# Performance work log

Hardware: AMD Instinct MI355X
Metric: run time of the kernel (lower is better)

Reference implementation:

```python
import jax, jax.numpy as jnp
import numpy as np

DEPTH = 6
N_EST = 16
IN_DIM = 512
N_CLASSES = 100
BATCH = 8192
N_NODES = 2 ** DEPTH - 1   # 63 internal nodes
N_LEAVES = 2 ** DEPTH      # 64 leaves


def entmax15(t):
    # Source's (nonstandard) entmax15: softmax(relu(t)**1.5)
    z = jax.nn.relu(t)
    return jax.nn.softmax(z ** 1.5, axis=-1)


def _leaf_paths():
    # Ancestor node index and branch bit for every (depth level j, leaf l),
    # exactly matching: idx = 2**(j-1) + l // 2**(depth-(j-1)) - 1
    #                   bit = (l // 2**(depth-j)) % 2
    l = np.arange(N_LEAVES)
    j = np.arange(1, DEPTH + 1)[:, None]
    idx = (2 ** (j - 1) + l[None, :] // (2 ** (DEPTH - (j - 1))) - 1).astype(np.int32)
    bits = ((l[None, :] // (2 ** (DEPTH - j))) % 2).astype(np.int32)
    return jnp.asarray(idx), jnp.asarray(bits)  # both (DEPTH, N_LEAVES)


def setup_inputs() -> dict:
    key = jax.random.key(0)
    kx, kT, kL = jax.random.split(key, 3)
    x = jax.random.normal(kx, (BATCH, IN_DIM), dtype=jnp.float32)
    T = jax.random.normal(kT, (N_EST, N_NODES, IN_DIM), dtype=jnp.float32)
    L = jax.random.normal(kL, (N_EST, N_LEAVES, N_CLASSES), dtype=jnp.float32)
    return {"x": x, "T": T, "L": L}


def reference(x, T, L):
    # Hard feature selection with straight-through: forward = hardmax(entmax15(T)),
    # backward = 0 (in the torch source, I = I - (I - hardmax(I)) kills the gradient).
    I_soft = entmax15(T)  # (E, N, D)
    I = jax.lax.stop_gradient(
        (I_soft == I_soft.max(axis=-1, keepdims=True)).astype(x.dtype)
    )
    # Per-node split decisions for all nodes at once.
    t_dot = jnp.einsum('end,end->en', T, I)          # (E, N) threshold value
    x_dot = jnp.einsum('bd,end->ben', x, I)          # (B, E, N) selected feature
    # s = s - (s - floor(s)) == floor(s); floor has zero gradient (matches torch).
    s = jnp.floor(t_dot[None, :, :] - x_dot)         # (B, E, N)

    idx, bits = _leaf_paths()                        # (DEPTH, N_LEAVES)
    sg = s[..., idx]                                 # (B, E, DEPTH, N_LEAVES)
    factors = jnp.where(bits[None, None] == 1, 1.0 - sg, sg)
    p = jnp.prod(factors, axis=2)                    # (B, E, N_LEAVES)

    # Leaf values, summed over the ensemble.
    y_hat = jnp.einsum('bel,elc->bc', p, L)          # (B, C)
    return jax.nn.softmax(y_hat, axis=-1)
```

## Files before the change

### kernel.cpp

```cpp
#include <hip/hip_runtime.h>
#include <hip/hip_bf16.h>
#include <math.h>

#define IN_DIM 512
#define NC 100
#define NN 63
#define NE 16
#define BATCH 8192
#define XP 516

typedef __attribute__((ext_vector_type(8))) short bf16x8;
typedef __attribute__((ext_vector_type(4))) float f32x4;

static __device__ __forceinline__ ushort bf16_bits(__hip_bfloat16 h) {
  union { __hip_bfloat16 b; ushort u; } cv; cv.b = h; return cv.u;
}

__global__ __launch_bounds__(256) void prep_kernel(
    const float* __restrict__ T, const float* __restrict__ L,
    ushort* __restrict__ Bfrag, float* __restrict__ tmax, int* __restrict__ dstar) {
  const int tid = threadIdx.x;
  const int bid = blockIdx.x;

  {
    const int i = bid * 256 + tid;
    const int j = i & 7;
    const int lane = (i >> 3) & 63;
    const int cf = (i >> 9) & 7;
    const int hl = (i >> 12) & 1;
    const int kc = i >> 13;
    const int k = kc * 32 + (lane >> 4) * 8 + j;
    const int c = cf * 16 + (lane & 15);
    const float val = (c < NC) ? L[(size_t)k * NC + c] : 0.0f;
    const __hip_bfloat16 hb = __float2bfloat16(val);
    ushort outv;
    if (hl == 0) {
      outv = bf16_bits(hb);
    } else {
      const __hip_bfloat16 lb = __float2bfloat16(val - __bfloat162float(hb));
      outv = bf16_bits(lb);
    }
    Bfrag[i] = outv;
  }

  if (bid < NE * NN && tid < 64) {
    const float4* row = reinterpret_cast<const float4*>(T + (size_t)bid * IN_DIM);
    const int lane = tid;
    float best = -INFINITY;
    int bidx = 0;
#pragma unroll
    for (int i = 0; i < 2; ++i) {
      const int f4 = lane + 64 * i;
      const float4 v = row[f4];
      const int base = f4 * 4;
      if (v.x > best) { best = v.x; bidx = base; }
      if (v.y > best) { best = v.y; bidx = base + 1; }
      if (v.z > best) { best = v.z; bidx = base + 2; }
      if (v.w > best) { best = v.w; bidx = base + 3; }
    }
#pragma unroll
    for (int off = 32; off; off >>= 1) {
      const float ov = __shfl_xor(best, off);
      const int oi = __shfl_xor(bidx, off);
      if (ov > best || (ov == best && oi < bidx)) { best = ov; bidx = oi; }
    }
    if (lane == 0) {
      tmax[bid] = best;
      dstar[bid] = bidx;
    }
  }
}

__global__ __launch_bounds__(256, 2) void forest_fused_kernel(
    const float* __restrict__ x, const ushort* __restrict__ Bfrag,
    const float* __restrict__ tmaxg, const int* __restrict__ dstarg,
    float* __restrict__ out) {
  __shared__ __align__(16) float xl[16 * XP];
  __shared__ float tl[NE * NN];
  __shared__ int dl[NE * NN];
  __shared__ __align__(16) float red[4 * 16 * 128];
  const int tid = threadIdx.x;
  const int b0 = blockIdx.x * 16;
  const int w = tid >> 6, lane = tid & 63;

  {
    const float4* xg = reinterpret_cast<const float4*>(x + (size_t)b0 * IN_DIM);
#pragma unroll
    for (int i = 0; i < 8; ++i) {
      const int idx = tid + i * 256;
      const int r = idx >> 7, c4 = idx & 127;
      *reinterpret_cast<float4*>(&xl[r * XP + c4 * 4]) = xg[r * 128 + c4];
    }
    for (int i = tid; i < NE * NN; i += 256) { tl[i] = tmaxg[i]; dl[i] = dstarg[i]; }
  }
  __syncthreads();

  const int r = lane & 15;
  const int lgq = lane >> 4;
  const float* xr = &xl[r * XP];
  const bf16x8* bf = reinterpret_cast<const bf16x8*>(Bfrag);

  f32x4 acc[8];
#pragma unroll
  for (int cf = 0; cf < 8; ++cf) acc[cf] = (f32x4)0.0f;

  for (int t = 0; t < 8; ++t) {
    const int kc = w * 8 + t;
    const int e = kc >> 1;
    const int lg = (kc & 1) * 4 + lgq;

    const size_t bbase = (size_t)kc * 1024;
    bf16x8 BH[8], BL[8];
#pragma unroll
    for (int cf = 0; cf < 8; ++cf) {
      BH[cf] = bf[bbase + (size_t)cf * 64 + lane];
      BL[cf] = bf[bbase + 512 + (size_t)cf * 64 + lane];
    }

    const float* te = &tl[e * NN];
    const int* de = &dl[e * NN];
    const float s1 = floorf(te[0] - xr[de[0]]);
    const int n2 = 1 + (lg >> 2), n3 = 3 + (lg >> 1), n4 = 7 + lg;
    const float s2 = floorf(te[n2] - xr[de[n2]]);
    const float s3 = floorf(te[n3] - xr[de[n3]]);
    const float s4 = floorf(te[n4] - xr[de[n4]]);
    const int n5 = 15 + 2 * lg, n6 = 31 + 4 * lg;
    const float s5a = floorf(te[n5] - xr[de[n5]]);
    const float s5b = floorf(te[n5 + 1] - xr[de[n5 + 1]]);
    const float s60 = floorf(te[n6] - xr[de[n6]]);
    const float s61 = floorf(te[n6 + 1] - xr[de[n6 + 1]]);
    const float s62 = floorf(te[n6 + 2] - xr[de[n6 + 2]]);
    const float s63 = floorf(te[n6 + 3] - xr[de[n6 + 3]]);

    const float f1 = ((lg >> 2) & 1) ? 1.0f - s1 : s1;
    const float f2 = ((lg >> 1) & 1) ? 1.0f - s2 : s2;
    const float f3 = (lg & 1) ? 1.0f - s3 : s3;
    const float stem = f1 * f2 * f3;
    const float qa = stem * s4, qb = stem * (1.0f - s4);
    const float w00 = qa * s5a, w01 = qa * (1.0f - s5a);
    const float w10 = qb * s5b, w11 = qb * (1.0f - s5b);
    float p[8];
    p[0] = w00 * s60; p[1] = w00 * (1.0f - s60);
    p[2] = w01 * s61; p[3] = w01 * (1.0f - s61);
    p[4] = w10 * s62; p[5] = w10 * (1.0f - s62);
    p[6] = w11 * s63; p[7] = w11 * (1.0f - s63);

    union { ushort u[8]; bf16x8 v; } H, Lo;
#pragma unroll
    for (int i2 = 0; i2 < 8; ++i2) {
      const __hip_bfloat16 hb = __float2bfloat16(p[i2]);
      const float hf = __bfloat162float(hb);
      H.u[i2] = bf16_bits(hb);
      Lo.u[i2] = bf16_bits(__float2bfloat16(p[i2] - hf));
    }
    const bf16x8 Ah = H.v, Al = Lo.v;

#pragma unroll
    for (int cf = 0; cf < 8; ++cf) {
      acc[cf] = __builtin_amdgcn_mfma_f32_16x16x32_bf16(Ah, BH[cf], acc[cf], 0, 0, 0);
      acc[cf] = __builtin_amdgcn_mfma_f32_16x16x32_bf16(Al, BH[cf], acc[cf], 0, 0, 0);
      acc[cf] = __builtin_amdgcn_mfma_f32_16x16x32_bf16(Ah, BL[cf], acc[cf], 0, 0, 0);
      acc[cf] = __builtin_amdgcn_mfma_f32_16x16x32_bf16(Al, BL[cf], acc[cf], 0, 0, 0);
    }
  }

  {
    const int rlo = (lane >> 4) * 4;
    const int cl = lane & 15;
#pragma unroll
    for (int cf = 0; cf < 8; ++cf)
#pragma unroll
      for (int jj = 0; jj < 4; ++jj)
        red[(w * 16 + rlo + jj) * 128 + cf * 16 + cl] = acc[cf][jj];
  }
  __syncthreads();

  const int rr = tid >> 4;
  const int cg = tid & 15;
  float v[8];
#pragma unroll
  for (int j = 0; j < 8; ++j) {
    const int c = cg * 8 + j;
    v[j] = red[(0 * 16 + rr) * 128 + c] + red[(1 * 16 + rr) * 128 + c] +
           red[(2 * 16 + rr) * 128 + c] + red[(3 * 16 + rr) * 128 + c];
  }
  float m = -INFINITY;
#pragma unroll
  for (int j = 0; j < 8; ++j)
    if (cg * 8 + j < NC) m = fmaxf(m, v[j]);
#pragma unroll
  for (int off = 1; off < 16; off <<= 1) m = fmaxf(m, __shfl_xor(m, off));
  float ev[8];
  float ss = 0.0f;
#pragma unroll
  for (int j = 0; j < 8; ++j) {
    ev[j] = (cg * 8 + j < NC) ? __expf(v[j] - m) : 0.0f;
    ss += ev[j];
  }
#pragma unroll
  for (int off = 1; off < 16; off <<= 1) ss += __shfl_xor(ss, off);
  const float inv = 1.0f / ss;
  float* orow = out + (size_t)(b0 + rr) * NC + cg * 8;
  if (cg < 12) {
    *reinterpret_cast<float4*>(orow) =
        make_float4(ev[0] * inv, ev[1] * inv, ev[2] * inv, ev[3] * inv);
    *reinterpret_cast<float4*>(orow + 4) =
        make_float4(ev[4] * inv, ev[5] * inv, ev[6] * inv, ev[7] * inv);
  } else if (cg == 12) {
    *reinterpret_cast<float4*>(orow) =
        make_float4(ev[0] * inv, ev[1] * inv, ev[2] * inv, ev[3] * inv);
  }
}

extern "C" void kernel_launch(void* const* d_in, const int* in_sizes, int n_in,
                              void* d_out, int out_size, void* d_ws, size_t ws_size,
                              hipStream_t stream) {
  const float* x = (const float*)d_in[0];
  const float* T = (const float*)d_in[1];
  const float* L = (const float*)d_in[2];
  float* out = (float*)d_out;

  char* ws = (char*)d_ws;
  ushort* Bfrag = (ushort*)ws;
  float* tmax = (float*)(ws + 524288);
  int* dstar = (int*)(ws + 528384);

  prep_kernel<<<1024, 256, 0, stream>>>(T, L, Bfrag, tmax, dstar);
  forest_fused_kernel<<<BATCH / 16, 256, 0, stream>>>(x, Bfrag, tmax, dstar, out);
}
```

Before: 23.98 us.

## Process 32 batch rows per block with 8 waves reusing B fragments

Each block now handles 32 batch rows with 512 threads (8 waves). Each wave covers half as many K-chunks but computes two 16-row tiles, so every B fragment loaded from global memory feeds MFMAs for both row tiles. This halves global traffic for the leaf-value fragments per output row and doubles the cross-wave reduction width. The costs are more shared memory (about 110KB per block, likely limiting occupancy to one block per CU), twice the accumulator registers, and a serialized two-pass epilogue with an extra barrier.

```diff
diff --git a/kernel.cpp b/kernel.cpp
--- a/kernel.cpp
+++ b/kernel.cpp
@@ -71,54 +71,38 @@
   }
 }
 
-__global__ __launch_bounds__(256, 2) void forest_fused_kernel(
+__global__ __launch_bounds__(512, 2) void forest_fused_kernel(
     const float* __restrict__ x, const ushort* __restrict__ Bfrag,
     const float* __restrict__ tmaxg, const int* __restrict__ dstarg,
     float* __restrict__ out) {
-  __shared__ __align__(16) float xl[16 * XP];
+  __shared__ __align__(16) float xl[32 * XP];
   __shared__ float tl[NE * NN];
   __shared__ int dl[NE * NN];
-  __shared__ __align__(16) float red[4 * 16 * 128];
+  __shared__ __align__(16) float red[8 * 16 * 128];
   const int tid = threadIdx.x;
-  const int b0 = blockIdx.x * 16;
+  const int b0 = blockIdx.x * 32;
   const int w = tid >> 6, lane = tid & 63;
 
   {
     const float4* xg = reinterpret_cast<const float4*>(x + (size_t)b0 * IN_DIM);
 #pragma unroll
     for (int i = 0; i < 8; ++i) {
-      const int idx = tid + i * 256;
+      const int idx = tid + i * 512;
       const int r = idx >> 7, c4 = idx & 127;
       *reinterpret_cast<float4*>(&xl[r * XP + c4 * 4]) = xg[r * 128 + c4];
     }
-    for (int i = tid; i < NE * NN; i += 256) { tl[i] = tmaxg[i]; dl[i] = dstarg[i]; }
+    for (int i = tid; i < NE * NN; i += 512) { tl[i] = tmaxg[i]; dl[i] = dstarg[i]; }
   }
   __syncthreads();
 
   const int r = lane & 15;
   const int lgq = lane >> 4;
-  const float* xr = &xl[r * XP];
+  const float* xr0 = &xl[r * XP];
+  const float* xr1 = &xl[(r + 16) * XP];
   const bf16x8* bf = reinterpret_cast<const bf16x8*>(Bfrag);
 
-  f32x4 acc[8];
-#pragma unroll
-  for (int cf = 0; cf < 8; ++cf) acc[cf] = (f32x4)0.0f;
-
-  for (int t = 0; t < 8; ++t) {
-    const int kc = w * 8 + t;
-    const int e = kc >> 1;
-    const int lg = (kc & 1) * 4 + lgq;
-
-    const size_t bbase = (size_t)kc * 1024;
-    bf16x8 BH[8], BL[8];
-#pragma unroll
-    for (int cf = 0; cf < 8; ++cf) {
-      BH[cf] = bf[bbase + (size_t)cf * 64 + lane];
-      BL[cf] = bf[bbase + 512 + (size_t)cf * 64 + lane];
-    }
-
-    const float* te = &tl[e * NN];
-    const int* de = &dl[e * NN];
+  auto agen = [&](const float* xr, int lg, const float* te, const int* de,
+                  bf16x8& Ah, bf16x8& Al) {
     const float s1 = floorf(te[0] - xr[de[0]]);
     const int n2 = 1 + (lg >> 2), n3 = 3 + (lg >> 1), n4 = 7 + lg;
     const float s2 = floorf(te[n2] - xr[de[n2]]);
@@ -131,7 +115,6 @@
     const float s61 = floorf(te[n6 + 1] - xr[de[n6 + 1]]);
     const float s62 = floorf(te[n6 + 2] - xr[de[n6 + 2]]);
     const float s63 = floorf(te[n6 + 3] - xr[de[n6 + 3]]);
-
     const float f1 = ((lg >> 2) & 1) ? 1.0f - s1 : s1;
     const float f2 = ((lg >> 1) & 1) ? 1.0f - s2 : s2;
     const float f3 = (lg & 1) ? 1.0f - s3 : s3;
@@ -144,7 +127,6 @@
     p[2] = w01 * s61; p[3] = w01 * (1.0f - s61);
     p[4] = w10 * s62; p[5] = w10 * (1.0f - s62);
     p[6] = w11 * s63; p[7] = w11 * (1.0f - s63);
-
     union { ushort u[8]; bf16x8 v; } H, Lo;
 #pragma unroll
     for (int i2 = 0; i2 < 8; ++i2) {
@@ -153,63 +135,95 @@
       H.u[i2] = bf16_bits(hb);
       Lo.u[i2] = bf16_bits(__float2bfloat16(p[i2] - hf));
     }
-    const bf16x8 Ah = H.v, Al = Lo.v;
-
+    Ah = H.v; Al = Lo.v;
+  };
+
+  f32x4 acc0[8], acc1[8];
+#pragma unroll
+  for (int cf = 0; cf < 8; ++cf) { acc0[cf] = (f32x4)0.0f; acc1[cf] = (f32x4)0.0f; }
+
+  for (int t = 0; t < 4; ++t) {
+    const int kc = w * 4 + t;
+    const int e = kc >> 1;
+    const int lg = (kc & 1) * 4 + lgq;
+
+    const size_t bbase = (size_t)kc * 1024;
+    bf16x8 BH[8], BL[8];
 #pragma unroll
     for (int cf = 0; cf < 8; ++cf) {
-      acc[cf] = __builtin_amdgcn_mfma_f32_16x16x32_bf16(Ah, BH[cf], acc[cf], 0, 0, 0);
-      acc[cf] = __builtin_amdgcn_mfma_f32_16x16x32_bf16(Al, BH[cf], acc[cf], 0, 0, 0);
-      acc[cf] = __builtin_amdgcn_mfma_f32_16x16x32_bf16(Ah, BL[cf], acc[cf], 0, 0, 0);
-      acc[cf] = __builtin_amdgcn_mfma_f32_16x16x32_bf16(Al, BL[cf], acc[cf], 0, 0, 0);
-    }
-  }
-
-  {
-    const int rlo = (lane >> 4) * 4;
-    const int cl = lane & 15;
+      BH[cf] = bf[bbase + (size_t)cf * 64 + lane];
+      BL[cf] = bf[bbase + 512 + (size_t)cf * 64 + lane];
+    }
+
+    const float* te = &tl[e * NN];
+    const int* de = &dl[e * NN];
+    bf16x8 Ah, Al;
+
+    agen(xr0, lg, te, de, Ah, Al);
+#pragma unroll
+    for (int cf = 0; cf < 8; ++cf) {
+      acc0[cf] = __builtin_amdgcn_mfma_f32_16x16x32_bf16(Ah, BH[cf], acc0[cf], 0, 0, 0);
+      acc0[cf] = __builtin_amdgcn_mfma_f32_16x16x32_bf16(Al, BH[cf], acc0[cf], 0, 0, 0);
+      acc0[cf] = __builtin_amdgcn_mfma_f32_16x16x32_bf16(Ah, BL[cf], acc0[cf], 0, 0, 0);
+      acc0[cf] = __builtin_amdgcn_mfma_f32_16x16x32_bf16(Al, BL[cf], acc0[cf], 0, 0, 0);
+    }
+    agen(xr1, lg, te, de, Ah, Al);
+#pragma unroll
+    for (int cf = 0; cf < 8; ++cf) {
+      acc1[cf] = __builtin_amdgcn_mfma_f32_16x16x32_bf16(Ah, BH[cf], acc1[cf], 0, 0, 0);
+      acc1[cf] = __builtin_amdgcn_mfma_f32_16x16x32_bf16(Al, BH[cf], acc1[cf], 0, 0, 0);
+      acc1[cf] = __builtin_amdgcn_mfma_f32_16x16x32_bf16(Ah, BL[cf], acc1[cf], 0, 0, 0);
+      acc1[cf] = __builtin_amdgcn_mfma_f32_16x16x32_bf16(Al, BL[cf], acc1[cf], 0, 0, 0);
+    }
+  }
+
+  const int rlo = (lane >> 4) * 4;
+  const int cl = lane & 15;
+  const int rr = tid >> 5;
+  const int cg = tid & 31;
+
+  auto epi = [&](const f32x4 (&ac)[8], int rowbase) {
 #pragma unroll
     for (int cf = 0; cf < 8; ++cf)
 #pragma unroll
       for (int jj = 0; jj < 4; ++jj)
-        red[(w * 16 + rlo + jj) * 128 + cf * 16 + cl] = acc[cf][jj];
-  }
+        red[(w * 16 + rlo + jj) * 128 + cf * 16 + cl] = ac[cf][jj];
+    __syncthreads();
+    float v[4];
+#pragma unroll
+    for (int j = 0; j < 4; ++j) {
+      const int c = cg * 4 + j;
+      float s = red[(0 * 16 + rr) * 128 + c];
+#pragma unroll
+      for (int pw = 1; pw < 8; ++pw) s += red[(pw * 16 + rr) * 128 + c];
+      v[j] = s;
+    }
+    float m = -INFINITY;
+#pragma unroll
+    for (int j = 0; j < 4; ++j)
+      if (cg * 4 + j < NC) m = fmaxf(m, v[j]);
+#pragma unroll
+    for (int off = 1; off < 32; off <<= 1) m = fmaxf(m, __shfl_xor(m, off));
+    float ev[4];
+    float ss = 0.0f;
+#pragma unroll
+    for (int j = 0; j < 4; ++j) {
+      ev[j] = (cg * 4 + j < NC) ? __expf(v[j] - m) : 0.0f;
+      ss += ev[j];
+    }
+#pragma unroll
+    for (int off = 1; off < 32; off <<= 1) ss += __shfl_xor(ss, off);
+    const float inv = 1.0f / ss;
+    if (cg < 25) {
+      float* orow = out + (size_t)(b0 + rowbase + rr) * NC + cg * 4;
+      *reinterpret_cast<float4*>(orow) =
+          make_float4(ev[0] * inv, ev[1] * inv, ev[2] * inv, ev[3] * inv);
+    }
+  };
+
+  epi(acc0, 0);
   __syncthreads();
-
-  const int rr = tid >> 4;
-  const int cg = tid & 15;
-  float v[8];
-#pragma unroll
-  for (int j = 0; j < 8; ++j) {
-    const int c = cg * 8 + j;
-    v[j] = red[(0 * 16 + rr) * 128 + c] + red[(1 * 16 + rr) * 128 + c] +
-           red[(2 * 16 + rr) * 128 + c] + red[(3 * 16 + rr) * 128 + c];
-  }
-  float m = -INFINITY;
-#pragma unroll
-  for (int j = 0; j < 8; ++j)
-    if (cg * 8 + j < NC) m = fmaxf(m, v[j]);
-#pragma unroll
-  for (int off = 1; off < 16; off <<= 1) m = fmaxf(m, __shfl_xor(m, off));
-  float ev[8];
-  float ss = 0.0f;
-#pragma unroll
-  for (int j = 0; j < 8; ++j) {
-    ev[j] = (cg * 8 + j < NC) ? __expf(v[j] - m) : 0.0f;
-    ss += ev[j];
-  }
-#pragma unroll
-  for (int off = 1; off < 16; off <<= 1) ss += __shfl_xor(ss, off);
-  const float inv = 1.0f / ss;
-  float* orow = out + (size_t)(b0 + rr) * NC + cg * 8;
-  if (cg < 12) {
-    *reinterpret_cast<float4*>(orow) =
-        make_float4(ev[0] * inv, ev[1] * inv, ev[2] * inv, ev[3] * inv);
-    *reinterpret_cast<float4*>(orow + 4) =
-        make_float4(ev[4] * inv, ev[5] * inv, ev[6] * inv, ev[7] * inv);
-  } else if (cg == 12) {
-    *reinterpret_cast<float4*>(orow) =
-        make_float4(ev[0] * inv, ev[1] * inv, ev[2] * inv, ev[3] * inv);
-  }
+  epi(acc1, 16);
 }
 
 extern "C" void kernel_launch(void* const* d_in, const int* in_sizes, int n_in,
@@ -226,5 +240,5 @@
   int* dstar = (int*)(ws + 528384);
 
   prep_kernel<<<1024, 256, 0, stream>>>(T, L, Bfrag, tmax, dstar);
-  forest_fused_kernel<<<BATCH / 16, 256, 0, stream>>>(x, Bfrag, tmax, dstar, out);
-}
+  forest_fused_kernel<<<BATCH / 32, 512, 0, stream>>>(x, Bfrag, tmax, dstar, out);
+}
```

After: 22.14 us. 1.08x faster.
